# Optimization experiments

Measured on AMD Instinct MI355X. Metric: run time of the kernel, lower is better.

Reference implementation:

```python
import jax, jax.numpy as jnp
import numpy as np
import math

B, T, C = 8, 1024, 1024
E, K = 8, 2
H = 4 * C


def new_gelu(x):
    # tanh-approx GELU, identical to the torch reference
    c = math.sqrt(2.0 / math.pi)
    return 0.5 * x * (1.0 + jnp.tanh(c * (x + 0.044715 * x ** 3)))


def setup_inputs() -> dict:
    key = jax.random.key(0)
    ks = jax.random.split(key, 4)
    x = jax.random.normal(ks[0], (B, T, C), dtype=jnp.float32)
    # router: nn.Linear(C, E, bias=False), weight [E, C], init std=0.02
    router_w = 0.02 * jax.random.normal(ks[1], (E, C), dtype=jnp.float32)
    # stacked expert MLP weights (bias=False): c_fc [E, C, H], c_proj [E, H, C]
    w_fc = 0.02 * jax.random.normal(ks[2], (E, C, H), dtype=jnp.float32)
    w_proj = 0.02 * jax.random.normal(ks[3], (E, H, C), dtype=jnp.float32)
    return {"x": x, "router_w": router_w, "w_fc": w_fc, "w_proj": w_proj}


def reference(x, router_w, w_fc, w_proj):
    n_expert = w_fc.shape[0]
    seq_rep = x.mean(axis=1)                                  # [B, C]
    router_logits = seq_rep @ router_w.T                      # [B, E]
    probs_full = jax.nn.softmax(router_logits.astype(jnp.float32), axis=-1)
    probs = probs_full.astype(x.dtype)
    weights, sel = jax.lax.top_k(probs, K)                    # [B, K]
    weights = weights / weights.sum(axis=-1, keepdims=True)

    # gather selected expert weights and run grouped dense MLPs
    w1 = w_fc[sel]                                            # [B, K, C, H]
    w2 = w_proj[sel]                                          # [B, K, H, C]
    h = new_gelu(jnp.einsum('btc,bkch->bkth', x, w1))         # [B, K, T, H]
    out_k = jnp.einsum('bkth,bkhc->bktc', h, w2)              # [B, K, T, C]
    final_output = jnp.einsum('bk,bktc->btc', weights, out_k)

    # load balancing loss
    Bf = jnp.asarray(x.shape[0], jnp.float32)
    expert_importance = probs_full.sum(axis=0) / Bf           # [E]
    is_assigned = jnp.zeros_like(probs_full).at[jnp.arange(x.shape[0])[:, None], sel].set(1.0)
    expert_load = is_assigned.sum(axis=0) / Bf                # [E]
    load_balancing_loss = n_expert * jnp.sum(expert_importance * expert_load)
    return final_output, load_balancing_loss
```

## Files before the change

### kernel.cpp

```cpp
#include <hip/hip_runtime.h>

#define B_ 8
#define T_ 1024
#define C_ 1024
#define E_ 8
#define H_ 4096

typedef float v4f __attribute__((ext_vector_type(4)));
typedef short v8s __attribute__((ext_vector_type(8)));

__device__ __forceinline__ unsigned short f2bf(float f) {
  union { float f; unsigned int u; } x; x.f = f;
  unsigned int r = x.u + 0x7fffu + ((x.u >> 16) & 1u);
  return (unsigned short)(r >> 16);
}

__device__ __forceinline__ void async_load16(const unsigned short* g, unsigned short* l) {
  __builtin_amdgcn_global_load_lds(
      (const __attribute__((address_space(1))) void*)g,
      (__attribute__((address_space(3))) void*)l, 16, 0, 0);
}


__global__ void k_meanpart(const float* __restrict__ x, float* __restrict__ part,
                           unsigned short* __restrict__ xb) {
  int b = blockIdx.x >> 3, tc = blockIdx.x & 7;
  int c4 = threadIdx.x * 4;
  const size_t base = (size_t)b * T_ * C_ + (size_t)tc * 128 * C_ + c4;
  const float* xp = x + base;
  v4f s = {0.f, 0.f, 0.f, 0.f};
  for (int t = 0; t < 128; ++t) {
    v4f v = *(const v4f*)(xp + (size_t)t * C_);
    s += v;
    ushort4 o;
    o.x = f2bf(v.x); o.y = f2bf(v.y); o.z = f2bf(v.z); o.w = f2bf(v.w);
    *(ushort4*)(xb + base + (size_t)t * C_) = o;
  }
  *(v4f*)(part + (size_t)(tc * B_ + b) * C_ + c4) = s;
}

__global__ void k_router(const float* __restrict__ part, const float* __restrict__ rw,
                         int* __restrict__ sel, float* __restrict__ wv,
                         float* __restrict__ loss_out) {
  __shared__ float seq[B_ * C_];
  __shared__ float pr[B_][E_];
  __shared__ int ss[B_][2];
  const int tid = threadIdx.x;
  for (int idx = tid; idx < B_ * C_; idx += 256) {
    float s = 0.f;
#pragma unroll
    for (int tc = 0; tc < 8; ++tc) s += part[(size_t)tc * B_ * C_ + idx];
    seq[idx] = s * (1.0f / T_);
  }
  __syncthreads();
  if (tid < B_ * E_) {
    int b = tid >> 3, e = tid & 7;
    float acc = 0.f;
    for (int c = 0; c < C_; ++c) acc += seq[b * C_ + c] * rw[e * C_ + c];
    pr[b][e] = acc;
  }
  __syncthreads();
  if (tid < B_) {
    int b = tid;
    float mx = pr[b][0];
#pragma unroll
    for (int e = 1; e < E_; ++e) mx = fmaxf(mx, pr[b][e]);
    float p[E_]; float sum = 0.f;
#pragma unroll
    for (int e = 0; e < E_; ++e) { p[e] = __expf(pr[b][e] - mx); sum += p[e]; }
    float inv = 1.0f / sum;
#pragma unroll
    for (int e = 0; e < E_; ++e) { p[e] *= inv; pr[b][e] = p[e]; }
    int i0 = 0;
#pragma unroll
    for (int e = 1; e < E_; ++e) if (p[e] > p[i0]) i0 = e;
    int i1 = (i0 == 0) ? 1 : 0;
#pragma unroll
    for (int e = 0; e < E_; ++e) if (e != i0 && p[e] > p[i1]) i1 = e;
    float s2 = p[i0] + p[i1];
    sel[b * 2 + 0] = i0; sel[b * 2 + 1] = i1;
    wv[b * 2 + 0] = p[i0] / s2; wv[b * 2 + 1] = p[i1] / s2;
    ss[b][0] = i0; ss[b][1] = i1;
  }
  __syncthreads();
  if (tid == 0) {
    float loss = 0.f;
    for (int e = 0; e < E_; ++e) {
      float imp = 0.f, ld = 0.f;
      for (int b = 0; b < B_; ++b) {
        imp += pr[b][e];
        ld += ((ss[b][0] == e) || (ss[b][1] == e)) ? 1.f : 0.f;
      }
      loss += (imp / (float)B_) * (ld / (float)B_);
    }
    loss_out[0] = loss * (float)E_;
  }
}

__global__ void k_transpose(const float* __restrict__ src, unsigned short* __restrict__ dst,
                            int R, int Cc) {
  __shared__ float tile[64][65];
  const size_t sl = (size_t)blockIdx.z * R * Cc;
  int c0 = blockIdx.x * 64, r0 = blockIdx.y * 64;
  int tx = threadIdx.x & 15, ty = threadIdx.x >> 4;
#pragma unroll
  for (int p = 0; p < 4; ++p) {
    int r = p * 16 + ty;
    v4f v = *(const v4f*)(src + sl + (size_t)(r0 + r) * Cc + c0 + tx * 4);
    tile[r][tx * 4 + 0] = v.x; tile[r][tx * 4 + 1] = v.y;
    tile[r][tx * 4 + 2] = v.z; tile[r][tx * 4 + 3] = v.w;
  }
  __syncthreads();
#pragma unroll
  for (int p = 0; p < 4; ++p) {
    int c = p * 16 + ty;
    int rr = tx * 4;
    ushort4 o;
    o.x = f2bf(tile[rr + 0][c]); o.y = f2bf(tile[rr + 1][c]);
    o.z = f2bf(tile[rr + 2][c]); o.w = f2bf(tile[rr + 3][c]);
    *(ushort4*)(dst + sl + (size_t)(c0 + c) * R + r0 + rr) = o;
  }
}


__device__ __forceinline__ void gemm_seg(const unsigned short* A, int lda,
                                         const unsigned short* Bt, int ldb,
                                         int Kd, int row0, int col0,
                                         unsigned short* As, unsigned short* Bs,
                                         v4f (&acc)[4][4]) {
  const int tid = threadIdx.x;
  const int lane = tid & 63;
  const int wave = __builtin_amdgcn_readfirstlane(tid >> 6);
  const int r = lane & 15, q = lane >> 4;
  const int wm = wave & 1, wn = wave >> 1;
  const int lrow = lane >> 2, lch = lane & 3;
  const bool doA = (wave < 2);
  const int jb = (wave & 1) * 4;
  const int gld = doA ? lda : ldb;
  const unsigned short* gbase =
      (doA ? (A + (size_t)row0 * lda) : (Bt + (size_t)col0 * ldb)) +
      (size_t)(jb * 16 + lrow) * gld + lch * 8;
  unsigned short* lbase = (doA ? As : Bs) + jb * 512;

  for (int kc = 0; kc < Kd; kc += 32) {
    const unsigned short* g = gbase + kc;
    async_load16(g + 0 * 16 * (size_t)gld, lbase + 0 * 512);
    async_load16(g + 1 * 16 * (size_t)gld, lbase + 1 * 512);
    async_load16(g + 2 * 16 * (size_t)gld, lbase + 2 * 512);
    async_load16(g + 3 * 16 * (size_t)gld, lbase + 3 * 512);
    __syncthreads();
    v8s af[4], bf[4];
#pragma unroll
    for (int i = 0; i < 4; ++i)
      af[i] = *(const v8s*)&As[(wm * 64 + i * 16 + r) * 32 + q * 8];
#pragma unroll
    for (int j = 0; j < 4; ++j)
      bf[j] = *(const v8s*)&Bs[(wn * 64 + j * 16 + r) * 32 + q * 8];
#pragma unroll
    for (int i = 0; i < 4; ++i)
#pragma unroll
      for (int j = 0; j < 4; ++j)
        acc[i][j] = __builtin_amdgcn_mfma_f32_16x16x32_bf16(af[i], bf[j], acc[i][j], 0, 0, 0);
    __syncthreads();
  }
}

__global__ __launch_bounds__(256, 4) void k_gemm1(
    const unsigned short* __restrict__ Xb, const unsigned short* __restrict__ Wfct,
    const int* __restrict__ sel, const float* __restrict__ wv,
    unsigned short* __restrict__ Hout) {
  __shared__ unsigned short SH[128 * 64];
  unsigned short* As = SH;
  unsigned short* Bs = SH + 128 * 32;
  const int bk = blockIdx.z;
  const int e = sel[bk];
  const float wgt = wv[bk];
  const int row0 = blockIdx.y * 128, col0 = blockIdx.x * 128;
  v4f acc[4][4];
#pragma unroll
  for (int i = 0; i < 4; ++i)
#pragma unroll
    for (int j = 0; j < 4; ++j) acc[i][j] = (v4f){0.f, 0.f, 0.f, 0.f};

  gemm_seg(Xb + (size_t)(bk >> 1) * T_ * C_, C_, Wfct + (size_t)e * H_ * C_, C_,
           C_, row0, col0, As, Bs, acc);

  const int tid = threadIdx.x;
  const int lane = tid & 63;
  const int wave = tid >> 6;
  const int r = lane & 15, q = lane >> 4;
  const int wm = wave & 1, wn = wave >> 1;
  unsigned short* Co = Hout + (size_t)bk * T_ * H_;
#pragma unroll
  for (int hh = 0; hh < 2; ++hh) {
    if (wm == hh) {
#pragma unroll
      for (int i = 0; i < 4; ++i)
#pragma unroll
        for (int j = 0; j < 4; ++j)
#pragma unroll
          for (int p = 0; p < 4; ++p) {
            int lr = i * 16 + q * 4 + p;
            int lc = wn * 64 + j * 16 + r;
            float u = acc[i][j][p];
            float y = 0.7978845608028654f * (u + 0.044715f * u * u * u);
            float t = 1.0f - 2.0f / (__expf(2.0f * y) + 1.0f);
            SH[lr * 128 + lc] = f2bf(0.5f * u * (1.0f + t) * wgt);
          }
    }
    __syncthreads();
#pragma unroll
    for (int it = 0; it < 4; ++it) {
      int idx = it * 256 + tid;
      int row = idx >> 4, ch = idx & 15;
      *(v8s*)&Co[(size_t)(row0 + hh * 64 + row) * H_ + col0 + ch * 8] =
          *(const v8s*)&SH[row * 128 + ch * 8];
    }
    __syncthreads();
  }
}

__global__ __launch_bounds__(256, 4) void k_gemm2(
    const unsigned short* __restrict__ Hin, const unsigned short* __restrict__ Wpt,
    const int* __restrict__ sel, float* __restrict__ P0, float* __restrict__ P1) {
  __shared__ unsigned short SH[128 * 64];
  unsigned short* As = SH;
  unsigned short* Bs = SH + 128 * 32;
  const int bk = blockIdx.z;
  const int b = bk >> 1, k = bk & 1;
  const int e = sel[bk];
  const int row0 = blockIdx.y * 128, col0 = blockIdx.x * 128;
  v4f acc[4][4];
#pragma unroll
  for (int i = 0; i < 4; ++i)
#pragma unroll
    for (int j = 0; j < 4; ++j) acc[i][j] = (v4f){0.f, 0.f, 0.f, 0.f};

  gemm_seg(Hin + (size_t)bk * T_ * H_, H_, Wpt + (size_t)e * C_ * H_, H_,
           H_, row0, col0, As, Bs, acc);

  const int lane = threadIdx.x & 63;
  const int wave = threadIdx.x >> 6;
  const int r = lane & 15, q = lane >> 4;
  const int wm = wave & 1, wn = wave >> 1;
  float* Co = (k == 0 ? P0 : P1) + (size_t)b * T_ * C_;
#pragma unroll
  for (int i = 0; i < 4; ++i) {
    int gr = row0 + wm * 64 + i * 16 + q * 4;
#pragma unroll
    for (int j = 0; j < 4; ++j) {
      int gc = col0 + wn * 64 + j * 16 + r;
#pragma unroll
      for (int p = 0; p < 4; ++p)
        Co[(size_t)(gr + p) * C_ + gc] = acc[i][j][p];
    }
  }
}

__global__ void k_add(float* __restrict__ out, const float* __restrict__ p1) {
  size_t i = ((size_t)blockIdx.x * 256 + threadIdx.x) * 4;
  v4f a = *(const v4f*)(out + i);
  v4f b = *(const v4f*)(p1 + i);
  a += b;
  *(v4f*)(out + i) = a;
}


extern "C" void kernel_launch(void* const* d_in, const int* in_sizes, int n_in,
                              void* d_out, int out_size, void* d_ws, size_t ws_size,
                              hipStream_t stream) {
  const float* x   = (const float*)d_in[0];
  const float* rw  = (const float*)d_in[1];
  const float* wfc = (const float*)d_in[2];
  const float* wpj = (const float*)d_in[3];
  float* out = (float*)d_out;
  char* ws = (char*)d_ws;

  float*          part = (float*)(ws + 0);
  int*            sel  = (int*)(ws + 262144);
  float*          wv   = (float*)(ws + 262144 + 64);
  unsigned short* xb   = (unsigned short*)(ws + 524288);
  unsigned short* wfct = (unsigned short*)(ws + 524288 + 16777216);
  unsigned short* wpjt = (unsigned short*)(ws + 524288 + 16777216 + 67108864);
  unsigned short* h    = (unsigned short*)(ws + 524288 + 16777216 + 2*67108864ll);
  float*          p1   = (float*)(ws + 524288);

  k_meanpart<<<dim3(B_ * 8), dim3(256), 0, stream>>>(x, part, xb);
  k_router<<<dim3(1), dim3(256), 0, stream>>>(part, rw, sel, wv,
                                              out + (size_t)B_ * T_ * C_);
  k_transpose<<<dim3(H_ / 64, C_ / 64, E_), dim3(256), 0, stream>>>(wfc, wfct, C_, H_);
  k_transpose<<<dim3(C_ / 64, H_ / 64, E_), dim3(256), 0, stream>>>(wpj, wpjt, H_, C_);

  k_gemm1<<<dim3(H_ / 128, T_ / 128, B_ * 2), dim3(256), 0, stream>>>(xb, wfct, sel, wv, h);
  k_gemm2<<<dim3(C_ / 128, T_ / 128, B_ * 2), dim3(256), 0, stream>>>(h, wpjt, sel, out, p1);
  k_add<<<dim3(B_ * T_ * C_ / 4 / 256), dim3(256), 0, stream>>>(out, p1);
}
```

Measured before the change: 795.9 us.

## Reorganize GEMM LDS tile layout, widen mean-reduction grid, parallelize router dot products

The GEMM staging now has each lane load one full row's 16-element k-chunk into a k-major LDS layout, replacing the old row-interleaved layout. MFMA fragment reads now come from contiguous 16-byte slots, which is meant to reduce LDS bank conflicts and make global loads per lane more sequential. Separately, the mean/convert kernel launches four times as many blocks over shorter time chunks to better fill the GPU, with workspace offsets enlarged to fit. The router dot products are split across all 256 threads with a small shared-memory reduction.

```diff
diff --git a/kernel.cpp b/kernel.cpp
--- a/kernel.cpp
+++ b/kernel.cpp
@@ -24,12 +24,12 @@
 
 __global__ void k_meanpart(const float* __restrict__ x, float* __restrict__ part,
                            unsigned short* __restrict__ xb) {
-  int b = blockIdx.x >> 3, tc = blockIdx.x & 7;
+  int b = blockIdx.x >> 5, tc = blockIdx.x & 31;
   int c4 = threadIdx.x * 4;
-  const size_t base = (size_t)b * T_ * C_ + (size_t)tc * 128 * C_ + c4;
+  const size_t base = (size_t)b * T_ * C_ + (size_t)tc * 32 * C_ + c4;
   const float* xp = x + base;
   v4f s = {0.f, 0.f, 0.f, 0.f};
-  for (int t = 0; t < 128; ++t) {
+  for (int t = 0; t < 32; ++t) {
     v4f v = *(const v4f*)(xp + (size_t)t * C_);
     s += v;
     ushort4 o;
@@ -43,22 +43,29 @@
                          int* __restrict__ sel, float* __restrict__ wv,
                          float* __restrict__ loss_out) {
   __shared__ float seq[B_ * C_];
+  __shared__ float red[B_ * E_][4];
   __shared__ float pr[B_][E_];
   __shared__ int ss[B_][2];
   const int tid = threadIdx.x;
   for (int idx = tid; idx < B_ * C_; idx += 256) {
     float s = 0.f;
 #pragma unroll
-    for (int tc = 0; tc < 8; ++tc) s += part[(size_t)tc * B_ * C_ + idx];
+    for (int tc = 0; tc < 32; ++tc) s += part[(size_t)tc * B_ * C_ + idx];
     seq[idx] = s * (1.0f / T_);
   }
   __syncthreads();
-  if (tid < B_ * E_) {
-    int b = tid >> 3, e = tid & 7;
+  {
+    int pair = tid >> 2, sub = tid & 3;
+    int b = pair >> 3, e = pair & 7;
     float acc = 0.f;
-    for (int c = 0; c < C_; ++c) acc += seq[b * C_ + c] * rw[e * C_ + c];
-    pr[b][e] = acc;
-  }
+    const float* sp = seq + b * C_ + sub * 256;
+    const float* wp = rw + e * C_ + sub * 256;
+    for (int c = 0; c < 256; ++c) acc += sp[c] * wp[c];
+    red[pair][sub] = acc;
+  }
+  __syncthreads();
+  if (tid < B_ * E_)
+    pr[tid >> 3][tid & 7] = red[tid][0] + red[tid][1] + red[tid][2] + red[tid][3];
   __syncthreads();
   if (tid < B_) {
     int b = tid;
@@ -133,29 +140,28 @@
   const int wave = __builtin_amdgcn_readfirstlane(tid >> 6);
   const int r = lane & 15, q = lane >> 4;
   const int wm = wave & 1, wn = wave >> 1;
-  const int lrow = lane >> 2, lch = lane & 3;
   const bool doA = (wave < 2);
-  const int jb = (wave & 1) * 4;
+  const int w = wave & 1;
   const int gld = doA ? lda : ldb;
-  const unsigned short* gbase =
+  const unsigned short* gp0 =
       (doA ? (A + (size_t)row0 * lda) : (Bt + (size_t)col0 * ldb)) +
-      (size_t)(jb * 16 + lrow) * gld + lch * 8;
-  unsigned short* lbase = (doA ? As : Bs) + jb * 512;
+      (size_t)lane * gld + w * 16;
+  const unsigned short* gp1 = gp0 + (size_t)64 * gld;
+  unsigned short* lb = (doA ? As : Bs) + w * 2048;
 
   for (int kc = 0; kc < Kd; kc += 32) {
-    const unsigned short* g = gbase + kc;
-    async_load16(g + 0 * 16 * (size_t)gld, lbase + 0 * 512);
-    async_load16(g + 1 * 16 * (size_t)gld, lbase + 1 * 512);
-    async_load16(g + 2 * 16 * (size_t)gld, lbase + 2 * 512);
-    async_load16(g + 3 * 16 * (size_t)gld, lbase + 3 * 512);
+    async_load16(gp0 + kc,     lb + 0 * 512);
+    async_load16(gp1 + kc,     lb + 1 * 512);
+    async_load16(gp0 + kc + 8, lb + 2 * 512);
+    async_load16(gp1 + kc + 8, lb + 3 * 512);
     __syncthreads();
     v8s af[4], bf[4];
 #pragma unroll
     for (int i = 0; i < 4; ++i)
-      af[i] = *(const v8s*)&As[(wm * 64 + i * 16 + r) * 32 + q * 8];
+      af[i] = *(const v8s*)&As[(q * 128 + wm * 64 + i * 16 + r) * 8];
 #pragma unroll
     for (int j = 0; j < 4; ++j)
-      bf[j] = *(const v8s*)&Bs[(wn * 64 + j * 16 + r) * 32 + q * 8];
+      bf[j] = *(const v8s*)&Bs[(q * 128 + wn * 64 + j * 16 + r) * 8];
 #pragma unroll
     for (int i = 0; i < 4; ++i)
 #pragma unroll
@@ -277,15 +283,15 @@
   char* ws = (char*)d_ws;
 
   float*          part = (float*)(ws + 0);
-  int*            sel  = (int*)(ws + 262144);
-  float*          wv   = (float*)(ws + 262144 + 64);
-  unsigned short* xb   = (unsigned short*)(ws + 524288);
-  unsigned short* wfct = (unsigned short*)(ws + 524288 + 16777216);
-  unsigned short* wpjt = (unsigned short*)(ws + 524288 + 16777216 + 67108864);
-  unsigned short* h    = (unsigned short*)(ws + 524288 + 16777216 + 2*67108864ll);
-  float*          p1   = (float*)(ws + 524288);
-
-  k_meanpart<<<dim3(B_ * 8), dim3(256), 0, stream>>>(x, part, xb);
+  int*            sel  = (int*)(ws + 1048576);
+  float*          wv   = (float*)(ws + 1048576 + 64);
+  unsigned short* xb   = (unsigned short*)(ws + 2097152);
+  unsigned short* wfct = (unsigned short*)(ws + 2097152 + 16777216);
+  unsigned short* wpjt = (unsigned short*)(ws + 2097152 + 16777216 + 67108864);
+  unsigned short* h    = (unsigned short*)(ws + 2097152 + 16777216 + 2*67108864ll);
+  float*          p1   = (float*)(ws + 2097152);
+
+  k_meanpart<<<dim3(B_ * 32), dim3(256), 0, stream>>>(x, part, xb);
   k_router<<<dim3(1), dim3(256), 0, stream>>>(part, rw, sel, wv,
                                               out + (size_t)B_ * T_ * C_);
   k_transpose<<<dim3(H_ / 64, C_ / 64, E_), dim3(256), 0, stream>>>(wfc, wfct, C_, H_);
```

After: 990.0 us. +24.4%, slower.
